# Performance work log

Hardware: AMD Instinct MI355X
Metric: run time of the kernel (lower is better)

## Reference

```python
import math
import jax, jax.numpy as jnp
import numpy as np

B, S, D, H, F, L = 32, 512, 512, 8, 2048, 4
DH = D // H
ALPHA = 1.0
LN_EPS = 1e-12


def setup_inputs() -> dict:
    key = jax.random.key(0)
    ks = jax.random.split(key, 24)
    n = jax.random.normal
    inp = {
        "hidden_states": n(ks[0], (B, S, D), dtype=jnp.float32),
        "position_bias": n(ks[1], (1, H, S, S), dtype=jnp.float32) * 0.02,
        "timestamp": jnp.sort(jax.random.randint(ks[2], (B, S), 0, 10_000_000), axis=-1).astype(jnp.int64),
        # per-layer stacked BERT params
        "Wq": n(ks[3], (L, D, D), dtype=jnp.float32) * 0.02,
        "bq": jnp.zeros((L, D), dtype=jnp.float32),
        "Wk": n(ks[4], (L, D, D), dtype=jnp.float32) * 0.02,
        "bk": jnp.zeros((L, D), dtype=jnp.float32),
        "Wv": n(ks[5], (L, D, D), dtype=jnp.float32) * 0.02,
        "bv": jnp.zeros((L, D), dtype=jnp.float32),
        "Wo": n(ks[6], (L, D, D), dtype=jnp.float32) * 0.02,
        "bo": jnp.zeros((L, D), dtype=jnp.float32),
        "ln1_g": jnp.ones((L, D), dtype=jnp.float32),
        "ln1_b": jnp.zeros((L, D), dtype=jnp.float32),
        "Wi": n(ks[7], (L, D, F), dtype=jnp.float32) * 0.02,
        "bi": jnp.zeros((L, F), dtype=jnp.float32),
        "Wf": n(ks[8], (L, F, D), dtype=jnp.float32) * 0.02,
        "bf": jnp.zeros((L, D), dtype=jnp.float32),
        "ln2_g": jnp.ones((L, D), dtype=jnp.float32),
        "ln2_b": jnp.zeros((L, D), dtype=jnp.float32),
    }
    return inp


def _layernorm(x, g, b):
    mu = jnp.mean(x, axis=-1, keepdims=True)
    var = jnp.mean(jnp.square(x - mu), axis=-1, keepdims=True)
    return (x - mu) * jax.lax.rsqrt(var + LN_EPS) * g + b


def _encoder(hidden_states, position_bias, timestamp,
             Wq, bq, Wk, bk, Wv, bv, Wo, bo, ln1_g, ln1_b,
             Wi, bi, Wf, bf, ln2_g, ln2_b):
    b_, s_, d_ = hidden_states.shape
    # lag-time scale (encoder path: raw timestamps, minutes)
    t = timestamp.astype(jnp.float32)
    lag = (t[:, :, None] - t[:, None, :]) / (60.0 * 1000.0)  # [B,S,S]
    scale = (math.sqrt(DH) - ALPHA / (jnp.maximum(lag, 0.0) + 1.0) + ALPHA)[:, None, :, :]  # [B,1,S,S]

    x = hidden_states
    for l in range(L):
        q = (x @ Wq[l] + bq[l]).reshape(b_, s_, H, DH)
        k = (x @ Wk[l] + bk[l]).reshape(b_, s_, H, DH)
        v = (x @ Wv[l] + bv[l]).reshape(b_, s_, H, DH)
        scores = jnp.einsum('bqhd,bkhd->bhqk', q, k) / scale + position_bias
        probs = jax.nn.softmax(scores, axis=-1)
        ctx = jnp.einsum('bhqk,bkhd->bqhd', probs, v).reshape(b_, s_, d_)
        attn = _layernorm(ctx @ Wo[l] + bo[l] + x, ln1_g[l], ln1_b[l])
        h = jax.nn.gelu(attn @ Wi[l] + bi[l], approximate=False)
        x = _layernorm(h @ Wf[l] + bf[l] + attn, ln2_g[l], ln2_b[l])
    return x


def reference(hidden_states, position_bias, timestamp,
              Wq, bq, Wk, bk, Wv, bv, Wo, bo, ln1_g, ln1_b,
              Wi, bi, Wf, bf, ln2_g, ln2_b):
    return _encoder(hidden_states, position_bias, timestamp,
                    Wq, bq, Wk, bk, Wv, bv, Wo, bo, ln1_g, ln1_b,
                    Wi, bi, Wf, bf, ln2_g, ln2_b)
```

## Files before the change

### kernel.cpp

```cpp
#include <hip/hip_runtime.h>
#include <stdint.h>

#define B_ 32
#define S_ 512
#define D_ 512
#define H_ 8
#define F_ 2048
#define L_ 4
#define DH_ 64
#define M_ (B_*S_)

typedef unsigned short u16;
typedef float f32x4 __attribute__((ext_vector_type(4)));
typedef short bf16x8 __attribute__((ext_vector_type(8)));

__device__ __forceinline__ u16 f2b(float f) {
  unsigned u = __float_as_uint(f);
  u += 0x7FFFu + ((u >> 16) & 1u);
  return (u16)(u >> 16);
}
__device__ __forceinline__ float b2f(u16 u) {
  return __uint_as_float((unsigned)u << 16);
}
__device__ __forceinline__ void gld16(const void* g, void* l) {
  __builtin_amdgcn_global_load_lds((__attribute__((address_space(1))) void*)(void*)g,
                                   (__attribute__((address_space(3))) void*)l, 16, 0, 0);
}
__device__ __forceinline__ f32x4 mfma16(bf16x8 a, bf16x8 b, f32x4 c) {
  return __builtin_amdgcn_mfma_f32_16x16x32_bf16(a, b, c, 0, 0, 0);
}
__device__ __forceinline__ float gelu_fast(float x) {
  float z = 0.7978845608028654f * fmaf(0.044715f * x, x * x, x);
  float e = __expf(2.0f * z);
  float t = 1.0f - 2.0f * __builtin_amdgcn_rcpf(e + 1.0f);
  return 0.5f * x * (1.0f + t);
}

#define LOG2E 1.4426950408889634f

__global__ __launch_bounds__(256) void transpose_w(const float* __restrict__ in,
                                                   u16* __restrict__ out, int R, int C) {
  __shared__ float tile[32][33];
  const int l = blockIdx.z;
  in  += (size_t)l * R * C;
  out += (size_t)l * R * C;
  const int c0 = blockIdx.x * 32, r0 = blockIdx.y * 32;
  const int tx = threadIdx.x, ty = threadIdx.y;
#pragma unroll
  for (int k = 0; k < 4; k++)
    tile[ty + 8*k][tx] = in[(size_t)(r0 + ty + 8*k) * C + c0 + tx];
  __syncthreads();
#pragma unroll
  for (int k = 0; k < 4; k++)
    out[(size_t)(c0 + ty + 8*k) * R + r0 + tx] = f2b(tile[tx][ty + 8*k]);
}

__global__ __launch_bounds__(256) void prep_x(const float* __restrict__ h,
                                              u16* __restrict__ xb) {
  int i = blockIdx.x * 256 + threadIdx.x;
  float4 v = ((const float4*)h)[i];
  ushort4 u; u.x = f2b(v.x); u.y = f2b(v.y); u.z = f2b(v.z); u.w = f2b(v.w);
  ((ushort4*)xb)[i] = u;
}

__global__ __launch_bounds__(256) void prep_pb(const float* __restrict__ pb,
                                               u16* __restrict__ out) {
  const int n0 = (blockIdx.x * 256 + threadIdx.x) * 4;
  const int rowbase = (n0 >> 9) << 9;
  const int nb = n0 & 511;
  const int blk = (nb >> 6) << 6;
  const int lr_ = (nb >> 2) & 15;
  const float* src = pb + rowbase + blk + lr_;
  ushort4 o;
  o.x = f2b(src[0]  * LOG2E);
  o.y = f2b(src[16] * LOG2E);
  o.z = f2b(src[32] * LOG2E);
  o.w = f2b(src[48] * LOG2E);
  ((ushort4*)out)[n0 >> 2] = o;
}

__global__ __launch_bounds__(256) void prep_inv(const int* __restrict__ ts,
                                                u16* __restrict__ invb) {
  const int b  = blockIdx.x >> 7;
  const int rg = blockIdx.x & 127;
  const int wid = threadIdx.x >> 6, lane = threadIdx.x & 63;
  const int i = rg * 4 + wid;
  const float ti = (float)ts[b*S_ + i];
  const int nblk = (lane >> 3) * 64;
  const int l8   = (lane & 7) * 8;
  u16 o[8];
#pragma unroll
  for (int e = 0; e < 8; e++) {
    const int no = l8 + e;
    const int j  = nblk + (no & 3) * 16 + ((no >> 2) & 15);
    float lag = fmaxf((ti - (float)ts[b*S_ + j]) * (1.0f/60000.0f), 0.0f);
    float iv  = (lag + 1.0f) * __builtin_amdgcn_rcpf(fmaf(lag, 9.0f, 8.0f)) * LOG2E;
    o[e] = (u16)(int)rintf((iv - 0.16f) * 524288.0f);
  }
  ushort4 w0 = {o[0], o[1], o[2], o[3]}, w1 = {o[4], o[5], o[6], o[7]};
  u16* out = invb + (((size_t)(b*S_ + i)) << 9) + lane*8;
  *(ushort4*)out       = w0;
  *(ushort4*)(out + 4) = w1;
}

__device__ __forceinline__ void gemm_core(
    const u16* __restrict__ A, const u16* __restrict__ BT,
    const int N, const int K,
    const float* __restrict__ bias, u16* __restrict__ outb, const int epi)
{
  __shared__ u16 As0[128*64], Bs0[128*64];
  __shared__ u16 As1[128*64], Bs1[128*64];
  const int tid = threadIdx.x;
  const int wid = tid >> 6, lane = tid & 63;
  const int wm = (wid >> 1) * 64, wn = (wid & 1) * 64;
  const int lr = lane & 15, quad = lane >> 4;
  const int m0 = blockIdx.x * 128, n0 = blockIdx.y * 128;
  const int l7 = lane & 7, l3 = lane >> 3;
  const int cc = (l7 ^ l3) * 8;
  const int f8 = lr & 7;

  f32x4 acc[4][4];
#pragma unroll
  for (int i = 0; i < 4; i++)
#pragma unroll
    for (int j = 0; j < 4; j++) acc[i][j] = (f32x4){0.f, 0.f, 0.f, 0.f};

  const u16* Ag = A  + (size_t)(m0 + wid*16 + l3)*K + cc;
  const u16* Bg = BT + (size_t)(n0 + l3*4 + wid)*K + cc;
  const int wo = wid * 1024;

  auto STAGE = [&](int k0, u16* AsB, u16* BsB) {
    u16* AsW = AsB + wo;
    u16* BsW = BsB + wo;
    gld16(Ag + k0,                 AsW);
    gld16(Ag + (size_t)8*K + k0,   AsW + 512);
    gld16(Ag + (size_t)64*K + k0,  AsW + 4096);
    gld16(Ag + (size_t)72*K + k0,  AsW + 4608);
    gld16(Bg + k0,                 BsW);
    gld16(Bg + (size_t)32*K + k0,  BsW + 512);
    gld16(Bg + (size_t)64*K + k0,  BsW + 4096);
    gld16(Bg + (size_t)96*K + k0,  BsW + 4608);
  };
  auto COMPUTE = [&](const u16* AsB, const u16* BsB) {
#pragma unroll
    for (int kh = 0; kh < 2; kh++) {
      bf16x8 af[4], bfr[4];
#pragma unroll
      for (int i = 0; i < 4; i++)
        af[i]  = *(const bf16x8*)(AsB + (wm + i*16 + lr)*64 + (((kh*4 + quad) ^ f8) * 8));
#pragma unroll
      for (int j = 0; j < 4; j++)
        bfr[j] = *(const bf16x8*)(BsB + (wn + j*16 + lr)*64 + (((kh*4 + quad) ^ f8) * 8));
#pragma unroll
      for (int i = 0; i < 4; i++)
#pragma unroll
        for (int j = 0; j < 4; j++)
          acc[i][j] = mfma16(af[i], bfr[j], acc[i][j]);
    }
  };

  const int NT = K >> 6;
  STAGE(0, As0, Bs0);
  __syncthreads();
  for (int t = 0; t < NT; t += 2) {
    STAGE((t + 1) << 6, As1, Bs1);
    COMPUTE(As0, Bs0);
    __syncthreads();
    if (t + 2 < NT) STAGE((t + 2) << 6, As0, Bs0);
    COMPUTE(As1, Bs1);
    __syncthreads();
  }

  const int nb = n0 + wn + lr*4;
  float4 b4 = *(const float4*)(bias + nb);
  float bn[4] = {b4.x, b4.y, b4.z, b4.w};

  if (epi == 3) {
#pragma unroll
    for (int i = 0; i < 4; i++) {
      const int m = m0 + wm + i*16 + quad*4;
      const int bb_ = m >> 9, sr = m & 511;
#pragma unroll
      for (int j = 0; j < 4; j++) {
        const int n = nb + j;
        const int hh = n >> 6, dd = n & 63;
        ushort4 o;
        o.x = f2b(acc[i][j][0] + bn[j]);
        o.y = f2b(acc[i][j][1] + bn[j]);
        o.z = f2b(acc[i][j][2] + bn[j]);
        o.w = f2b(acc[i][j][3] + bn[j]);
        *(ushort4*)(outb + (((size_t)((bb_*H_ + hh)*DH_ + dd)) << 9) + sr) = o;
      }
    }
  } else if (epi == 2) {
#pragma unroll
    for (int i = 0; i < 4; i++) {
#pragma unroll
      for (int r = 0; r < 4; r++) {
        const size_t m = (size_t)(m0 + wm + i*16 + quad*4 + r);
        ushort4 o;
        o.x = f2b(gelu_fast(acc[i][0][r] + bn[0]));
        o.y = f2b(gelu_fast(acc[i][1][r] + bn[1]));
        o.z = f2b(gelu_fast(acc[i][2][r] + bn[2]));
        o.w = f2b(gelu_fast(acc[i][3][r] + bn[3]));
        *(ushort4*)(outb + m*N + nb) = o;
      }
    }
  } else {
#pragma unroll
    for (int i = 0; i < 4; i++) {
#pragma unroll
      for (int r = 0; r < 4; r++) {
        const size_t m = (size_t)(m0 + wm + i*16 + quad*4 + r);
        ushort4 o;
        o.x = f2b(acc[i][0][r] + bn[0]);
        o.y = f2b(acc[i][1][r] + bn[1]);
        o.z = f2b(acc[i][2][r] + bn[2]);
        o.w = f2b(acc[i][3][r] + bn[3]);
        *(ushort4*)(outb + m*N + nb) = o;
      }
    }
  }
}

__global__ __launch_bounds__(256) void gemm_kernel(
    const u16* A, const u16* BT, int N, int K,
    const float* bias, u16* outb, int epi)
{
  gemm_core(A, BT, N, K, bias, outb, epi);
}

__global__ __launch_bounds__(256) void gemm_qkv_kernel(
    const u16* A, const u16* BTq, size_t zstride, int K,
    const float* b0, const float* b1, const float* b2,
    u16* out0, u16* out1, u16* out2)
{
  const int z = blockIdx.z;
  const u16* BT = BTq + (size_t)z * zstride;
  const float* bias = (z == 0) ? b0 : (z == 1) ? b1 : b2;
  u16* outb = (z == 0) ? out0 : (z == 1) ? out1 : out2;
  gemm_core(A, BT, 512, K, bias, outb, (z == 2) ? 3 : 0);
}

__global__ __launch_bounds__(256) void gemm64_kernel(
    const u16* __restrict__ A, const u16* __restrict__ BT,
    const int N, const int K,
    const float* __restrict__ bias, const u16* __restrict__ resb,
    float* __restrict__ outf)
{
  __shared__ u16 As0[64*64], Bs0[128*64];
  __shared__ u16 As1[64*64], Bs1[128*64];
  const int tid = threadIdx.x;
  const int wid = tid >> 6, lane = tid & 63;
  const int wm = (wid >> 1) * 32, wn = (wid & 1) * 64;
  const int lr = lane & 15, quad = lane >> 4;
  const int m0 = blockIdx.x * 64, n0 = blockIdx.y * 128;
  const int l7 = lane & 7, l3 = lane >> 3;
  const int cc = (l7 ^ l3) * 8;
  const int f8 = lr & 7;

  f32x4 acc[2][4];
#pragma unroll
  for (int i = 0; i < 2; i++)
#pragma unroll
    for (int j = 0; j < 4; j++) acc[i][j] = (f32x4){0.f, 0.f, 0.f, 0.f};

  const u16* Ag = A  + (size_t)(m0 + wid*8 + l3)*K + cc;
  const u16* Bg = BT + (size_t)(n0 + l3*4 + wid)*K + cc;

  auto STAGE = [&](int k0, u16* AsB, u16* BsB) {
    u16* AsW = AsB + wid*512;
    u16* BsW = BsB + wid*1024;
    gld16(Ag + k0,                AsW);
    gld16(Ag + (size_t)32*K + k0, AsW + 2048);
    gld16(Bg + k0,                 BsW);
    gld16(Bg + (size_t)32*K + k0,  BsW + 512);
    gld16(Bg + (size_t)64*K + k0,  BsW + 4096);
    gld16(Bg + (size_t)96*K + k0,  BsW + 4608);
  };
  auto COMPUTE = [&](const u16* AsB, const u16* BsB) {
#pragma unroll
    for (int kh = 0; kh < 2; kh++) {
      bf16x8 af[2], bfr[4];
#pragma unroll
      for (int i = 0; i < 2; i++)
        af[i]  = *(const bf16x8*)(AsB + (wm + i*16 + lr)*64 + (((kh*4 + quad) ^ f8) * 8));
#pragma unroll
      for (int j = 0; j < 4; j++)
        bfr[j] = *(const bf16x8*)(BsB + (wn + j*16 + lr)*64 + (((kh*4 + quad) ^ f8) * 8));
#pragma unroll
      for (int i = 0; i < 2; i++)
#pragma unroll
        for (int j = 0; j < 4; j++)
          acc[i][j] = mfma16(af[i], bfr[j], acc[i][j]);
    }
  };

  const int NT = K >> 6;
  STAGE(0, As0, Bs0);
  __syncthreads();
  for (int t = 0; t < NT; t += 2) {
    STAGE((t + 1) << 6, As1, Bs1);
    COMPUTE(As0, Bs0);
    __syncthreads();
    if (t + 2 < NT) STAGE((t + 2) << 6, As0, Bs0);
    COMPUTE(As1, Bs1);
    __syncthreads();
  }

  const int nb = n0 + wn + lr*4;
  float4 b4 = *(const float4*)(bias + nb);
  float bn[4] = {b4.x, b4.y, b4.z, b4.w};

#pragma unroll
  for (int i = 0; i < 2; i++) {
#pragma unroll
    for (int r = 0; r < 4; r++) {
      const size_t m = (size_t)(m0 + wm + i*16 + quad*4 + r);
      ushort4 rq = *(const ushort4*)(resb + m*N + nb);
      float4 ov;
      ov.x = acc[i][0][r] + bn[0] + b2f(rq.x);
      ov.y = acc[i][1][r] + bn[1] + b2f(rq.y);
      ov.z = acc[i][2][r] + bn[2] + b2f(rq.z);
      ov.w = acc[i][3][r] + bn[3] + b2f(rq.w);
      *(float4*)(outf + m*N + nb) = ov;
    }
  }
}

__global__ __launch_bounds__(256) void ln_kernel(
    const float* __restrict__ y, const float* __restrict__ g, const float* __restrict__ bta,
    float* __restrict__ outf, u16* __restrict__ outb)
{
  const int lane = threadIdx.x & 63;
  const int row = blockIdx.x*4 + (threadIdx.x >> 6);
  const float* yr = y + (size_t)row*D_ + lane*8;
  float4 a0 = *(const float4*)yr;
  float4 a1 = *(const float4*)(yr + 4);
  float v[8] = {a0.x, a0.y, a0.z, a0.w, a1.x, a1.y, a1.z, a1.w};
  float s = 0.f;
#pragma unroll
  for (int e = 0; e < 8; e++) s += v[e];
#pragma unroll
  for (int m = 1; m < 64; m <<= 1) s += __shfl_xor(s, m);
  const float mu = s * (1.0f/512.0f);
  float q = 0.f;
#pragma unroll
  for (int e = 0; e < 8; e++) { float d = v[e] - mu; q += d*d; }
#pragma unroll
  for (int m = 1; m < 64; m <<= 1) q += __shfl_xor(q, m);
  const float rs = rsqrtf(q * (1.0f/512.0f) + 1e-12f);
  float4 g0 = *(const float4*)(g + lane*8);
  float4 g1 = *(const float4*)(g + lane*8 + 4);
  float4 b0 = *(const float4*)(bta + lane*8);
  float4 b1 = *(const float4*)(bta + lane*8 + 4);
  float gg[8] = {g0.x, g0.y, g0.z, g0.w, g1.x, g1.y, g1.z, g1.w};
  float bb[8] = {b0.x, b0.y, b0.z, b0.w, b1.x, b1.y, b1.z, b1.w};
  float o[8];
#pragma unroll
  for (int e = 0; e < 8; e++) o[e] = (v[e] - mu) * rs * gg[e] + bb[e];
  if (outf) {
    float4 w0 = {o[0], o[1], o[2], o[3]}, w1 = {o[4], o[5], o[6], o[7]};
    *(float4*)(outf + (size_t)row*D_ + lane*8)     = w0;
    *(float4*)(outf + (size_t)row*D_ + lane*8 + 4) = w1;
  }
  ushort4 u0 = {f2b(o[0]), f2b(o[1]), f2b(o[2]), f2b(o[3])};
  ushort4 u1 = {f2b(o[4]), f2b(o[5]), f2b(o[6]), f2b(o[7])};
  *(ushort4*)(outb + (size_t)row*D_ + lane*8)     = u0;
  *(ushort4*)(outb + (size_t)row*D_ + lane*8 + 4) = u1;
}

__global__ __launch_bounds__(256, 4) void attn_kernel(
    const u16* __restrict__ qb, const u16* __restrict__ kb, const u16* __restrict__ vt,
    const u16* __restrict__ pb16, const u16* __restrict__ invb, u16* __restrict__ cb)
{
  __shared__ u16 QPs[64*64];
  __shared__ u16 Ks[64*64], Vs[64*64], PBs[64*64], INVs[64*64];
  const int b = blockIdx.x, it = blockIdx.y, h = blockIdx.z;
  const int i0 = it * 64;
  const int tid = threadIdx.x, wid = tid >> 6, lane = tid & 63;
  const int lr = lane & 15, quad = lane >> 4;
  const int l7 = lane & 7, l3 = lane >> 3;
  const int cc = (l7 ^ l3) * 8;
  const int f8 = lr & 7;
  const int rr = wid*8 + l3;

  const u16* qg  = qb + ((size_t)(b*S_ + i0))*D_ + h*DH_;
  const u16* kg  = kb + ((size_t)b*S_)*D_ + h*DH_;
  const u16* vg  = vt + ((size_t)(b*H_ + h)*DH_)*S_;
  const u16* pbg = pb16 + ((size_t)(h*S_ + i0))*S_;
  const u16* ivg = invb + ((size_t)(b*S_ + i0))*S_;

  gld16(qg + (size_t)rr*D_ + cc,        QPs + wid*512);
  gld16(qg + (size_t)(rr+32)*D_ + cc,   QPs + 2048 + wid*512);
  __syncthreads();

  bf16x8 aq0 = *(const bf16x8*)(QPs + (wid*16 + lr)*64 + ((quad ^ f8) * 8));
  bf16x8 aq1 = *(const bf16x8*)(QPs + (wid*16 + lr)*64 + (((quad ^ f8) ^ 4) * 8));
  u16* Pw = QPs + wid*1024;

  f32x4 O[4]; float lacc[4];
#pragma unroll
  for (int dt = 0; dt < 4; dt++) O[dt] = (f32x4){0.f, 0.f, 0.f, 0.f};
#pragma unroll
  for (int r = 0; r < 4; r++) lacc[r] = 0.f;
  const int lrh = lr >> 3;

  for (int t8 = 0; t8 < 8; t8++) {
    const int j0 = t8 * 64;
    gld16(kg + (size_t)(j0+rr)*D_ + cc,       Ks   + wid*512);
    gld16(kg + (size_t)(j0+rr+32)*D_ + cc,    Ks   + 2048 + wid*512);
    gld16(vg + (size_t)rr*S_ + j0 + cc,       Vs   + wid*512);
    gld16(vg + (size_t)(rr+32)*S_ + j0 + cc,  Vs   + 2048 + wid*512);
    gld16(pbg + (size_t)rr*S_ + j0 + cc,      PBs  + wid*512);
    gld16(pbg + (size_t)(rr+32)*S_ + j0 + cc, PBs  + 2048 + wid*512);
    gld16(ivg + (size_t)rr*S_ + j0 + cc,      INVs + wid*512);
    gld16(ivg + (size_t)(rr+32)*S_ + j0 + cc, INVs + 2048 + wid*512);
    __syncthreads();

    f32x4 s[4];
#pragma unroll
    for (int jt = 0; jt < 4; jt++) {
      const u16* kr = Ks + (jt*16 + lr)*64;
      bf16x8 bk0 = *(const bf16x8*)(kr + ((quad ^ f8) * 8));
      bf16x8 bk1 = *(const bf16x8*)(kr + (((quad ^ f8) ^ 4) * 8));
      f32x4 z = (f32x4){0.f, 0.f, 0.f, 0.f};
      z = mfma16(aq0, bk0, z);
      z = mfma16(aq1, bk1, z);
      s[jt] = z;
    }
#pragma unroll
    for (int r = 0; r < 4; r++) {
      const int rowl = quad*4 + r;
      const int r7 = rowl & 7;
      const int tbase = (wid*16 + rowl)*64 + ((((lr >> 1) ^ r7) << 3) | ((lr & 1) << 2));
      ushort4 ivq = *(const ushort4*)(INVs + tbase);
      ushort4 pbq = *(const ushort4*)(PBs + tbase);
      const u16 ive[4] = {ivq.x, ivq.y, ivq.z, ivq.w};
      const u16 pbe[4] = {pbq.x, pbq.y, pbq.z, pbq.w};
      const int pbase = rowl*64;
      float pa = 0.f;
#pragma unroll
      for (int jt = 0; jt < 4; jt++) {
        float iv  = fmaf((float)ive[jt], 0x1p-19f, 0.16f);
        float pbf = b2f(pbe[jt]);
        float p = __builtin_amdgcn_exp2f(fmaf(s[jt][r], iv, pbf));
        pa += p;
        const int idx = (((jt*2 + lrh) ^ r7) * 8) + l7;
        Pw[pbase + idx] = f2b(p);
      }
      lacc[r] += pa;
    }
    bf16x8 ap0 = *(const bf16x8*)(Pw + lr*64 + ((quad ^ f8) * 8));
    bf16x8 ap1 = *(const bf16x8*)(Pw + lr*64 + (((quad ^ f8) ^ 4) * 8));
#pragma unroll
    for (int dt = 0; dt < 4; dt++) {
      const u16* vr = Vs + (dt*16 + lr)*64;
      bf16x8 bv0 = *(const bf16x8*)(vr + ((quad ^ f8) * 8));
      bf16x8 bv1 = *(const bf16x8*)(vr + (((quad ^ f8) ^ 4) * 8));
      O[dt] = mfma16(ap0, bv0, O[dt]);
      O[dt] = mfma16(ap1, bv1, O[dt]);
    }
    __syncthreads();
  }

#pragma unroll
  for (int r = 0; r < 4; r++) {
    float sum = lacc[r];
#pragma unroll
    for (int m = 1; m < 16; m <<= 1) sum += __shfl_xor(sum, m);
    const float inv = __builtin_amdgcn_rcpf(sum);
    const size_t row = (size_t)(b*S_ + i0 + wid*16 + quad*4 + r);
#pragma unroll
    for (int dt = 0; dt < 4; dt++)
      cb[row*D_ + h*DH_ + dt*16 + lr] = f2b(O[dt][r] * inv);
  }
}

extern "C" void kernel_launch(void* const* d_in, const int* in_sizes, int n_in,
                              void* d_out, int out_size, void* d_ws, size_t ws_size,
                              hipStream_t stream)
{
  const float* hidden = (const float*)d_in[0];
  const float* pbias  = (const float*)d_in[1];
  const int*   ts     = (const int*)d_in[2];
  const float* Wq = (const float*)d_in[3];   const float* bq  = (const float*)d_in[4];
  const float* Wk = (const float*)d_in[5];   const float* bk  = (const float*)d_in[6];
  const float* Wv = (const float*)d_in[7];   const float* bv  = (const float*)d_in[8];
  const float* Wo = (const float*)d_in[9];   const float* bo  = (const float*)d_in[10];
  const float* l1g = (const float*)d_in[11]; const float* l1b = (const float*)d_in[12];
  const float* Wi = (const float*)d_in[13];  const float* bi  = (const float*)d_in[14];
  const float* Wf = (const float*)d_in[15];  const float* bfw = (const float*)d_in[16];
  const float* l2g = (const float*)d_in[17]; const float* l2b = (const float*)d_in[18];

  char* w = (char*)d_ws;
  u16* xb    = (u16*)w; w += (size_t)M_*D_*2;
  u16* qb    = (u16*)w; w += (size_t)M_*D_*2;
  u16* kbuf  = (u16*)w; w += (size_t)M_*D_*2;
  u16* vtw   = (u16*)w; w += (size_t)M_*D_*2;
  u16* cbuf  = (u16*)w; w += (size_t)M_*D_*2;
  u16* attnb = (u16*)w; w += (size_t)M_*D_*2;
  float* yf  = (float*)w; w += (size_t)M_*D_*4;
  u16* WqkvT = (u16*)w; w += (size_t)3*L_*D_*D_*2;
  u16* WoT   = (u16*)w; w += (size_t)L_*D_*D_*2;
  u16* WiT   = (u16*)w; w += (size_t)L_*D_*F_*2;
  u16* WfT   = (u16*)w; w += (size_t)L_*F_*D_*2;
  u16* pbb   = (u16*)w; w += (size_t)H_*S_*S_*2;
  u16* invb  = (u16*)w; w += (size_t)B_*S_*S_*2;
  u16* hb    = qb;

  float* x = (float*)d_out;

  const size_t WD = (size_t)D_*D_;
  const size_t WF = (size_t)D_*F_;
  dim3 tb(32, 8);

  transpose_w<<<dim3(16,16,L_), tb, 0, stream>>>(Wq, WqkvT,           D_, D_);
  transpose_w<<<dim3(16,16,L_), tb, 0, stream>>>(Wk, WqkvT + L_*WD,   D_, D_);
  transpose_w<<<dim3(16,16,L_), tb, 0, stream>>>(Wv, WqkvT + 2*L_*WD, D_, D_);
  transpose_w<<<dim3(16,16,L_), tb, 0, stream>>>(Wo, WoT,             D_, D_);
  transpose_w<<<dim3(64,16,L_), tb, 0, stream>>>(Wi, WiT,             D_, F_);
  transpose_w<<<dim3(16,64,L_), tb, 0, stream>>>(Wf, WfT,             F_, D_);
  prep_x<<<dim3(8192), dim3(256), 0, stream>>>(hidden, xb);
  prep_pb<<<dim3(H_*S_*S_/1024), dim3(256), 0, stream>>>(pbias, pbb);
  prep_inv<<<dim3(B_*S_/4), dim3(256), 0, stream>>>(ts, invb);

  for (int l = 0; l < L_; l++) {
    gemm_qkv_kernel<<<dim3(128,4,3), dim3(256), 0, stream>>>(
        xb, WqkvT + l*WD, (size_t)L_*WD, D_,
        bq + l*D_, bk + l*D_, bv + l*D_, qb, kbuf, vtw);
    attn_kernel<<<dim3(B_,8,H_), dim3(256), 0, stream>>>(qb, kbuf, vtw, pbb, invb, cbuf);
    gemm64_kernel<<<dim3(256,4), dim3(256), 0, stream>>>(
        cbuf, WoT + l*WD, D_, D_, bo + l*D_, xb, yf);
    ln_kernel<<<dim3(4096), dim3(256), 0, stream>>>(yf, l1g + l*D_, l1b + l*D_,
                                                    (float*)nullptr, attnb);
    gemm_kernel<<<dim3(128,16), dim3(256), 0, stream>>>(
        attnb, WiT + l*WF, F_, D_, bi + l*F_, hb, 2);
    gemm64_kernel<<<dim3(256,4), dim3(256), 0, stream>>>(
        hb, WfT + l*WF, D_, F_, bfw + l*D_, attnb, yf);
    ln_kernel<<<dim3(4096), dim3(256), 0, stream>>>(yf, l2g + l*D_, l2b + l*D_,
                                                    (l == 3) ? x : (float*)nullptr, xb);
  }
}
```

Baseline: 1.089 ms.

## Fuse output-projection and FFN-down GEMMs with residual add and LayerNorm

Replaces the 64x128-tile GEMM plus separate LayerNorm kernel with one kernel in which each 512-thread block computes a full 64x512 row tile, adds bias and residual, and performs the LayerNorm in-block. Row statistics come from wave shuffles plus a small shared-memory reduction that reuses the A staging buffer. This removes the fp32 intermediate buffer round-trip and two kernel launches per layer. In exchange the grid shrinks to 256 blocks with much larger shared-memory use (about 144KB) and more accumulators per thread, which may limit occupancy. Variance is computed as E[y^2]-mu^2, which can be less accurate than the two-pass form.

After: 978.9 us. -10.1%, faster.

```diff
diff --git a/kernel.cpp b/kernel.cpp
--- a/kernel.cpp
+++ b/kernel.cpp
@@ -242,56 +242,55 @@
   gemm_core(A, BT, 512, K, bias, outb, (z == 2) ? 3 : 0);
 }
 
-__global__ __launch_bounds__(256) void gemm64_kernel(
-    const u16* __restrict__ A, const u16* __restrict__ BT,
-    const int N, const int K,
+__global__ __launch_bounds__(512, 2) void gemm_ln_kernel(
+    const u16* __restrict__ A, const u16* __restrict__ BT, const int K,
     const float* __restrict__ bias, const u16* __restrict__ resb,
-    float* __restrict__ outf)
+    const float* __restrict__ g, const float* __restrict__ bta,
+    float* __restrict__ outf, u16* __restrict__ outb)
 {
-  __shared__ u16 As0[64*64], Bs0[128*64];
-  __shared__ u16 As1[64*64], Bs1[128*64];
+  __shared__ u16 As0[64*64],  As1[64*64];
+  __shared__ u16 Bs0[512*64], Bs1[512*64];
+  float (*red)[8] = (float(*)[8])(void*)As0;
   const int tid = threadIdx.x;
   const int wid = tid >> 6, lane = tid & 63;
-  const int wm = (wid >> 1) * 32, wn = (wid & 1) * 64;
+  const int wr = wid >> 2, wc = wid & 3;
+  const int wm = wr * 32;
   const int lr = lane & 15, quad = lane >> 4;
-  const int m0 = blockIdx.x * 64, n0 = blockIdx.y * 128;
+  const int m0 = blockIdx.x * 64;
   const int l7 = lane & 7, l3 = lane >> 3;
   const int cc = (l7 ^ l3) * 8;
   const int f8 = lr & 7;
 
-  f32x4 acc[2][4];
+  f32x4 acc[2][8];
 #pragma unroll
   for (int i = 0; i < 2; i++)
 #pragma unroll
-    for (int j = 0; j < 4; j++) acc[i][j] = (f32x4){0.f, 0.f, 0.f, 0.f};
+    for (int j = 0; j < 8; j++) acc[i][j] = (f32x4){0.f, 0.f, 0.f, 0.f};
 
   const u16* Ag = A  + (size_t)(m0 + wid*8 + l3)*K + cc;
-  const u16* Bg = BT + (size_t)(n0 + l3*4 + wid)*K + cc;
+  const u16* Bg = BT + (size_t)(wid*64 + l3*4)*K + cc;
 
   auto STAGE = [&](int k0, u16* AsB, u16* BsB) {
-    u16* AsW = AsB + wid*512;
-    u16* BsW = BsB + wid*1024;
-    gld16(Ag + k0,                AsW);
-    gld16(Ag + (size_t)32*K + k0, AsW + 2048);
-    gld16(Bg + k0,                 BsW);
-    gld16(Bg + (size_t)32*K + k0,  BsW + 512);
-    gld16(Bg + (size_t)64*K + k0,  BsW + 4096);
-    gld16(Bg + (size_t)96*K + k0,  BsW + 4608);
+    gld16(Ag + k0, AsB + wid*512);
+    u16* bw = BsB + wid*4096;
+#pragma unroll
+    for (int ld = 0; ld < 8; ld++)
+      gld16(Bg + (size_t)(32*(ld & 1) + (ld >> 1))*K + k0, bw + ld*512);
   };
   auto COMPUTE = [&](const u16* AsB, const u16* BsB) {
 #pragma unroll
     for (int kh = 0; kh < 2; kh++) {
-      bf16x8 af[2], bfr[4];
+      bf16x8 af[2], bfr[8];
 #pragma unroll
       for (int i = 0; i < 2; i++)
         af[i]  = *(const bf16x8*)(AsB + (wm + i*16 + lr)*64 + (((kh*4 + quad) ^ f8) * 8));
 #pragma unroll
-      for (int j = 0; j < 4; j++)
-        bfr[j] = *(const bf16x8*)(BsB + (wn + j*16 + lr)*64 + (((kh*4 + quad) ^ f8) * 8));
+      for (int j = 0; j < 8; j++)
+        bfr[j] = *(const bf16x8*)(BsB + (wc*128 + j*16 + lr)*64 + (((kh*4 + quad) ^ f8) * 8));
 #pragma unroll
       for (int i = 0; i < 2; i++)
 #pragma unroll
-        for (int j = 0; j < 4; j++)
+        for (int j = 0; j < 8; j++)
           acc[i][j] = mfma16(af[i], bfr[j], acc[i][j]);
     }
   };
@@ -308,66 +307,76 @@
     __syncthreads();
   }
 
-  const int nb = n0 + wn + lr*4;
-  float4 b4 = *(const float4*)(bias + nb);
-  float bn[4] = {b4.x, b4.y, b4.z, b4.w};
-
+  const int c0 = wc*128 + lr*4;
+  float4 bA = *(const float4*)(bias + c0);
+  float4 bB = *(const float4*)(bias + c0 + 64);
+  float sum[2][4], ssq[2][4];
 #pragma unroll
   for (int i = 0; i < 2; i++) {
 #pragma unroll
     for (int r = 0; r < 4; r++) {
-      const size_t m = (size_t)(m0 + wm + i*16 + quad*4 + r);
-      ushort4 rq = *(const ushort4*)(resb + m*N + nb);
-      float4 ov;
-      ov.x = acc[i][0][r] + bn[0] + b2f(rq.x);
-      ov.y = acc[i][1][r] + bn[1] + b2f(rq.y);
-      ov.z = acc[i][2][r] + bn[2] + b2f(rq.z);
-      ov.w = acc[i][3][r] + bn[3] + b2f(rq.w);
-      *(float4*)(outf + m*N + nb) = ov;
-    }
-  }
-}
-
-__global__ __launch_bounds__(256) void ln_kernel(
-    const float* __restrict__ y, const float* __restrict__ g, const float* __restrict__ bta,
-    float* __restrict__ outf, u16* __restrict__ outb)
-{
-  const int lane = threadIdx.x & 63;
-  const int row = blockIdx.x*4 + (threadIdx.x >> 6);
-  const float* yr = y + (size_t)row*D_ + lane*8;
-  float4 a0 = *(const float4*)yr;
-  float4 a1 = *(const float4*)(yr + 4);
-  float v[8] = {a0.x, a0.y, a0.z, a0.w, a1.x, a1.y, a1.z, a1.w};
-  float s = 0.f;
-#pragma unroll
-  for (int e = 0; e < 8; e++) s += v[e];
-#pragma unroll
-  for (int m = 1; m < 64; m <<= 1) s += __shfl_xor(s, m);
-  const float mu = s * (1.0f/512.0f);
-  float q = 0.f;
-#pragma unroll
-  for (int e = 0; e < 8; e++) { float d = v[e] - mu; q += d*d; }
-#pragma unroll
-  for (int m = 1; m < 64; m <<= 1) q += __shfl_xor(q, m);
-  const float rs = rsqrtf(q * (1.0f/512.0f) + 1e-12f);
-  float4 g0 = *(const float4*)(g + lane*8);
-  float4 g1 = *(const float4*)(g + lane*8 + 4);
-  float4 b0 = *(const float4*)(bta + lane*8);
-  float4 b1 = *(const float4*)(bta + lane*8 + 4);
-  float gg[8] = {g0.x, g0.y, g0.z, g0.w, g1.x, g1.y, g1.z, g1.w};
-  float bb[8] = {b0.x, b0.y, b0.z, b0.w, b1.x, b1.y, b1.z, b1.w};
-  float o[8];
-#pragma unroll
-  for (int e = 0; e < 8; e++) o[e] = (v[e] - mu) * rs * gg[e] + bb[e];
-  if (outf) {
-    float4 w0 = {o[0], o[1], o[2], o[3]}, w1 = {o[4], o[5], o[6], o[7]};
-    *(float4*)(outf + (size_t)row*D_ + lane*8)     = w0;
-    *(float4*)(outf + (size_t)row*D_ + lane*8 + 4) = w1;
-  }
-  ushort4 u0 = {f2b(o[0]), f2b(o[1]), f2b(o[2]), f2b(o[3])};
-  ushort4 u1 = {f2b(o[4]), f2b(o[5]), f2b(o[6]), f2b(o[7])};
-  *(ushort4*)(outb + (size_t)row*D_ + lane*8)     = u0;
-  *(ushort4*)(outb + (size_t)row*D_ + lane*8 + 4) = u1;
+      const size_t rowg = (size_t)(m0 + wm + i*16 + quad*4 + r);
+      ushort4 q0 = *(const ushort4*)(resb + rowg*D_ + c0);
+      ushort4 q1 = *(const ushort4*)(resb + rowg*D_ + c0 + 64);
+      acc[i][0][r] += bA.x + b2f(q0.x);
+      acc[i][1][r] += bA.y + b2f(q0.y);
+      acc[i][2][r] += bA.z + b2f(q0.z);
+      acc[i][3][r] += bA.w + b2f(q0.w);
+      acc[i][4][r] += bB.x + b2f(q1.x);
+      acc[i][5][r] += bB.y + b2f(q1.y);
+      acc[i][6][r] += bB.z + b2f(q1.z);
+      acc[i][7][r] += bB.w + b2f(q1.w);
+      float s = 0.f, q = 0.f;
+#pragma unroll
+      for (int j = 0; j < 8; j++) { float y = acc[i][j][r]; s += y; q += y*y; }
+#pragma unroll
+      for (int m = 1; m < 16; m <<= 1) { s += __shfl_xor(s, m); q += __shfl_xor(q, m); }
+      sum[i][r] = s; ssq[i][r] = q;
+    }
+  }
+  if (lr == 0) {
+#pragma unroll
+    for (int i = 0; i < 2; i++)
+#pragma unroll
+      for (int r = 0; r < 4; r++) {
+        const int rl = wm + i*16 + quad*4 + r;
+        red[rl][wc*2]     = sum[i][r];
+        red[rl][wc*2 + 1] = ssq[i][r];
+      }
+  }
+  __syncthreads();
+
+  float4 gA = *(const float4*)(g + c0);
+  float4 gB = *(const float4*)(g + c0 + 64);
+  float4 aA = *(const float4*)(bta + c0);
+  float4 aB = *(const float4*)(bta + c0 + 64);
+  float gg[8] = {gA.x, gA.y, gA.z, gA.w, gB.x, gB.y, gB.z, gB.w};
+  float bb[8] = {aA.x, aA.y, aA.z, aA.w, aB.x, aB.y, aB.z, aB.w};
+#pragma unroll
+  for (int i = 0; i < 2; i++) {
+#pragma unroll
+    for (int r = 0; r < 4; r++) {
+      const int rl = wm + i*16 + quad*4 + r;
+      const size_t rowg = (size_t)(m0 + rl);
+      float4 p0 = *(const float4*)&red[rl][0];
+      float4 p1 = *(const float4*)&red[rl][4];
+      const float mu = (p0.x + p0.z + p1.x + p1.z) * (1.0f/512.0f);
+      const float eq = (p0.y + p0.w + p1.y + p1.w) * (1.0f/512.0f);
+      const float rs = rsqrtf(fmaxf(eq - mu*mu, 0.0f) + 1e-12f);
+      float o[8];
+#pragma unroll
+      for (int j = 0; j < 8; j++) o[j] = (acc[i][j][r] - mu) * rs * gg[j] + bb[j];
+      ushort4 w0 = {f2b(o[0]), f2b(o[1]), f2b(o[2]), f2b(o[3])};
+      ushort4 w1 = {f2b(o[4]), f2b(o[5]), f2b(o[6]), f2b(o[7])};
+      *(ushort4*)(outb + rowg*D_ + c0)      = w0;
+      *(ushort4*)(outb + rowg*D_ + c0 + 64) = w1;
+      if (outf) {
+        float4 f0 = {o[0], o[1], o[2], o[3]}, f1 = {o[4], o[5], o[6], o[7]};
+        *(float4*)(outf + rowg*D_ + c0)      = f0;
+        *(float4*)(outf + rowg*D_ + c0 + 64) = f1;
+      }
+    }
+  }
 }
 
 __global__ __launch_bounds__(256, 4) void attn_kernel(
@@ -500,7 +509,6 @@
   u16* vtw   = (u16*)w; w += (size_t)M_*D_*2;
   u16* cbuf  = (u16*)w; w += (size_t)M_*D_*2;
   u16* attnb = (u16*)w; w += (size_t)M_*D_*2;
-  float* yf  = (float*)w; w += (size_t)M_*D_*4;
   u16* WqkvT = (u16*)w; w += (size_t)3*L_*D_*D_*2;
   u16* WoT   = (u16*)w; w += (size_t)L_*D_*D_*2;
   u16* WiT   = (u16*)w; w += (size_t)L_*D_*F_*2;
@@ -530,15 +538,13 @@
         xb, WqkvT + l*WD, (size_t)L_*WD, D_,
         bq + l*D_, bk + l*D_, bv + l*D_, qb, kbuf, vtw);
     attn_kernel<<<dim3(B_,8,H_), dim3(256), 0, stream>>>(qb, kbuf, vtw, pbb, invb, cbuf);
-    gemm64_kernel<<<dim3(256,4), dim3(256), 0, stream>>>(
-        cbuf, WoT + l*WD, D_, D_, bo + l*D_, xb, yf);
-    ln_kernel<<<dim3(4096), dim3(256), 0, stream>>>(yf, l1g + l*D_, l1b + l*D_,
-                                                    (float*)nullptr, attnb);
+    gemm_ln_kernel<<<dim3(256), dim3(512), 0, stream>>>(
+        cbuf, WoT + l*WD, D_, bo + l*D_, xb,
+        l1g + l*D_, l1b + l*D_, (float*)nullptr, attnb);
     gemm_kernel<<<dim3(128,16), dim3(256), 0, stream>>>(
         attnb, WiT + l*WF, F_, D_, bi + l*F_, hb, 2);
-    gemm64_kernel<<<dim3(256,4), dim3(256), 0, stream>>>(
-        hb, WfT + l*WF, D_, F_, bfw + l*D_, attnb, yf);
-    ln_kernel<<<dim3(4096), dim3(256), 0, stream>>>(yf, l2g + l*D_, l2b + l*D_,
-                                                    (l == 3) ? x : (float*)nullptr, xb);
-  }
-}
+    gemm_ln_kernel<<<dim3(256), dim3(512), 0, stream>>>(
+        hb, WfT + l*WF, F_, bfw + l*D_, attnb,
+        l2g + l*D_, l2b + l*D_, (l == 3) ? x : (float*)nullptr, xb);
+  }
+}
```
